# Optimization experiments

Measured on AMD Instinct MI355X. Metric: run time of the kernel, lower is better.

## Reference

```python
import jax, jax.numpy as jnp
import numpy as np

B, S, D = 4, 2048, 512
H, DK = 8, 64
FFN = 2048
LEFT, CHUNK, RIGHT = 512, 128, 128
EPS = 1e-5


def _emformer_mask():
    # True = disallowed. Each query attends to its own chunk, LEFT keys before
    # the chunk start, and RIGHT keys after the chunk end.
    idx = jnp.arange(S)
    cs = (idx // CHUNK) * CHUNK                      # chunk start per query
    j = idx[None, :]
    allowed = (j >= cs[:, None] - LEFT) & (j < cs[:, None] + CHUNK + RIGHT)
    return jnp.broadcast_to(~allowed, (B, 1, S, S))


def _ln(x, g, b):
    m = jnp.mean(x, axis=-1, keepdims=True)
    v = jnp.var(x, axis=-1, keepdims=True)
    return (x - m) * jax.lax.rsqrt(v + EPS) * g + b


def setup_inputs() -> dict:
    key = jax.random.key(0)
    ks = jax.random.split(key, 8)
    w = lambda k, shp: jax.random.normal(k, shp, dtype=jnp.float32) * 0.02
    return {
        "x": jax.random.normal(ks[0], (B, S, D), dtype=jnp.float32),
        "mask": _emformer_mask(),
        "ln_in_g": jnp.ones((D,), jnp.float32), "ln_in_b": jnp.zeros((D,), jnp.float32),
        "wq": w(ks[1], (D, D)), "bq": jnp.zeros((D,), jnp.float32),
        "wk": w(ks[2], (D, D)), "bk": jnp.zeros((D,), jnp.float32),
        "wv": w(ks[3], (D, D)), "bv": jnp.zeros((D,), jnp.float32),
        "ln1_g": jnp.ones((D,), jnp.float32), "ln1_b": jnp.zeros((D,), jnp.float32),
        "w1": w(ks[4], (D, FFN)), "b1": jnp.zeros((FFN,), jnp.float32),
        "w2": w(ks[5], (FFN, D)), "b2": jnp.zeros((D,), jnp.float32),
        "ln2_g": jnp.ones((D,), jnp.float32), "ln2_b": jnp.zeros((D,), jnp.float32),
    }


def reference(x, mask, ln_in_g, ln_in_b, wq, bq, wk, bk, wv, bv,
              ln1_g, ln1_b, w1, b1, w2, b2, ln2_g, ln2_b):
    h = _ln(x, ln_in_g, ln_in_b)                                  # [B,S,D]
    q = (h @ wq + bq).reshape(B, S, H, DK).transpose(0, 2, 1, 3)   # [B,H,S,DK]
    k = (h @ wk + bk).reshape(B, S, H, DK).transpose(0, 2, 1, 3)
    v = (h @ wv + bv).reshape(B, S, H, DK).transpose(0, 2, 1, 3)
    scores = jnp.einsum("bhqd,bhkd->bhqk", q, k) / np.sqrt(DK).astype(np.float32)
    scores = jnp.where(mask, -jnp.inf, scores)
    probs = jax.nn.softmax(scores, axis=-1)
    probs = jnp.where(mask, 0.0, probs)                           # masked_fill after softmax
    out = jnp.einsum("bhqk,bhkd->bhqd", probs, v)
    out = out.transpose(0, 2, 1, 3).reshape(B, S, D)
    attn_out = out + h                                            # residual uses post-LN input
    o = _ln(attn_out, ln1_g, ln1_b)
    o = (o @ w1 + b1) @ w2 + b2 + attn_out                        # NOTE: no activation in source
    return _ln(o, ln2_g, ln2_b)
```

## Files before the change

### kernel.cpp

```cpp
#include <hip/hip_runtime.h>
#include <stdint.h>

#define B_ 4
#define S_ 2048
#define D_ 512
#define H_ 8
#define FFN_ 2048
#define M_ (B_*S_)

typedef unsigned short u16;
typedef __attribute__((ext_vector_type(8))) __bf16 bf16x8;
typedef __attribute__((ext_vector_type(8))) u16 u16x8;
typedef __attribute__((ext_vector_type(4))) u16 u16x4;
typedef __attribute__((ext_vector_type(4))) float f32x4;

__device__ __forceinline__ u16 f2bf(float f) {
  uint32_t u = __builtin_bit_cast(uint32_t, f);
  u += 0x7FFFu + ((u >> 16) & 1u);
  return (u16)(u >> 16);
}
__device__ __forceinline__ bf16x8 ldfrag(const u16* p) {
  return __builtin_bit_cast(bf16x8, *(const u16x8*)p);
}
__device__ __forceinline__ void gld16(const void* g, void* l) {
  __builtin_amdgcn_global_load_lds(
      (const __attribute__((address_space(1))) void*)g,
      (__attribute__((address_space(3))) void*)l, 16, 0, 0);
}
template <int N>
__device__ __forceinline__ void wait_vm_barrier() {
  if constexpr (N == 0)      asm volatile("s_waitcnt vmcnt(0)\n\ts_barrier" ::: "memory");
  else if constexpr (N == 3) asm volatile("s_waitcnt vmcnt(3)\n\ts_barrier" ::: "memory");
  else if constexpr (N == 4) asm volatile("s_waitcnt vmcnt(4)\n\ts_barrier" ::: "memory");
  else if constexpr (N == 6) asm volatile("s_waitcnt vmcnt(6)\n\ts_barrier" ::: "memory");
  else if constexpr (N == 8) asm volatile("s_waitcnt vmcnt(8)\n\ts_barrier" ::: "memory");
}

__global__ __launch_bounds__(256)
void prep(const float* __restrict__ wq, const float* __restrict__ wk,
          const float* __restrict__ wv, const float* __restrict__ w1,
          const float* __restrict__ w2, const float* __restrict__ bq,
          const float* __restrict__ bk, const float* __restrict__ bv,
          u16* __restrict__ wqkvt, u16* __restrict__ w1t,
          u16* __restrict__ w2t, float* __restrict__ bqkv) {
  int id = blockIdx.x, tid = threadIdx.x;
  if (id >= 2816) {
    int i = (id - 2816) * 256 + tid;
    bqkv[i] = i < 512 ? bq[i] : (i < 1024 ? bk[i - 512] : bv[i - 1024]);
    return;
  }
  __shared__ float t[32][33];
  const float* W; u16* dst; int K, N, bx, by;
  if (id < 768) {
    int z = id >> 8, r = id & 255;
    W = z == 0 ? wq : (z == 1 ? wk : wv);
    dst = wqkvt + (size_t)z * 512 * 512; K = 512; N = 512;
    bx = r & 15; by = r >> 4;
  } else if (id < 1792) {
    int r = id - 768; W = w1; dst = w1t; K = 512; N = 2048;
    bx = r & 63; by = r >> 6;
  } else {
    int r = id - 1792; W = w2; dst = w2t; K = 2048; N = 512;
    bx = r & 15; by = r >> 4;
  }
  int n0 = bx * 32, k0 = by * 32, x = tid & 31, y = tid >> 5;
#pragma unroll
  for (int r = 0; r < 4; r++) t[y + 8*r][x] = W[(size_t)(k0 + y + 8*r) * N + n0 + x];
  __syncthreads();
#pragma unroll
  for (int r = 0; r < 4; r++) dst[(size_t)(n0 + y + 8*r) * K + k0 + x] = f2bf(t[x][y + 8*r]);
}

template <bool OUT32, bool OUT16, int NX>
__global__ __launch_bounds__(128)
void ln_k(const float* __restrict__ x, const float* __restrict__ g,
          const float* __restrict__ bta, float* __restrict__ y32,
          u16* __restrict__ y16, const u16* __restrict__ p1,
          const u16* __restrict__ p2, const u16* __restrict__ p3) {
  int row = blockIdx.x;
  int t = threadIdx.x;
  const float* xr = x + (size_t)row * 512;
  f32x4 v = *(const f32x4*)(xr + t * 4);
  if constexpr (NX >= 1) {
    u16x4 a = *(const u16x4*)(p1 + (size_t)row * 512 + t * 4);
#pragma unroll
    for (int j = 0; j < 4; j++) v[j] += __builtin_bit_cast(float, (uint32_t)a[j] << 16);
  }
  if constexpr (NX >= 2) {
    u16x4 a = *(const u16x4*)(p2 + (size_t)row * 512 + t * 4);
#pragma unroll
    for (int j = 0; j < 4; j++) v[j] += __builtin_bit_cast(float, (uint32_t)a[j] << 16);
  }
  if constexpr (NX >= 3) {
    u16x4 a = *(const u16x4*)(p3 + (size_t)row * 512 + t * 4);
#pragma unroll
    for (int j = 0; j < 4; j++) v[j] += __builtin_bit_cast(float, (uint32_t)a[j] << 16);
  }
  float s = v.x + v.y + v.z + v.w;
  float s2 = v.x*v.x + v.y*v.y + v.z*v.z + v.w*v.w;
#pragma unroll
  for (int m = 32; m; m >>= 1) { s += __shfl_xor(s, m); s2 += __shfl_xor(s2, m); }
  __shared__ float p[4];
  int wv = t >> 6;
  if ((t & 63) == 0) { p[wv] = s; p[2 + wv] = s2; }
  __syncthreads();
  s = p[0] + p[1]; s2 = p[2] + p[3];
  float mean = s * (1.f / 512.f);
  float var = s2 * (1.f / 512.f) - mean * mean;
  float rs = rsqrtf(var + 1e-5f);
#pragma unroll
  for (int j = 0; j < 4; j++) {
    float o = (v[j] - mean) * rs * g[t*4 + j] + bta[t*4 + j];
    if constexpr (OUT32) y32[(size_t)row * 512 + t*4 + j] = o;
    if constexpr (OUT16) y16[(size_t)row * 512 + t*4 + j] = f2bf(o);
  }
}

template <int NTW, int NCOL, int KSPLIT, bool RESID, bool OUT32, bool OUT16>
__global__ __launch_bounds__(256)
void gemm_db(const u16* __restrict__ A, const u16* __restrict__ Bt,
             const float* __restrict__ bias, int K, int N,
             const float* resid, float* C32, u16* __restrict__ C16,
             u16* __restrict__ C16b, u16* __restrict__ C16c) {
  __shared__ __align__(16) u16 As[3][128 * 32];
  __shared__ __align__(16) u16 Bs[3][NTW * 1024];
  const int tid = threadIdx.x;
  const int wave = tid >> 6, lane = tid & 63;
  const int l15 = lane & 15, quad = lane >> 4;
  const int wm = wave >> 1, wn = wave & 1;

  int lin = blockIdx.x;
  int kh = 0;
  if constexpr (KSPLIT > 1) {
    const int nblk = (M_ / 128) * NCOL;
    kh = lin / nblk;
    lin -= kh * nblk;
  }
  const int rpx = (M_ / 128) / 8;
  const int xcd = lin & 7, local = lin >> 3;
  const int row0 = (xcd * rpx + local / NCOL) * 128;
  const int col0 = (local % NCOL) * (NTW * 32);
  const int klen = K / KSPLIT;
  const int kstart = kh * klen;

  f32x4 acc[4][NTW];
#pragma unroll
  for (int i = 0; i < 4; i++)
#pragma unroll
    for (int j = 0; j < NTW; j++) acc[i][j] = (f32x4){0.f, 0.f, 0.f, 0.f};

  const int lr = lane >> 2;
  const int lc = ((lane & 3) ^ ((lane >> 3) & 3)) * 8;
  const u16* aG0 = A + (size_t)(row0 + (wave * 2) * 16 + lr) * K + lc;
  const u16* aG1 = A + (size_t)(row0 + (wave * 2 + 1) * 16 + lr) * K + lc;
  const int aO0 = (wave * 2) * 512 + lane * 8;
  const int aO1 = (wave * 2 + 1) * 512 + lane * 8;
  const u16* bG[NTW / 2];
  int bO[NTW / 2];
#pragma unroll
  for (int i = 0; i < NTW / 2; i++) {
    int ch = wave * (NTW / 2) + i;
    bG[i] = Bt + (size_t)(col0 + ch * 16 + lr) * K + lc;
    bO[i] = ch * 512 + lane * 8;
  }
  const int rsw = (l15 >> 1) & 3;
  constexpr int L = 2 + NTW / 2;

  auto issue = [&](int kof, int buf) {
    gld16(aG0 + kof, &As[buf][aO0]);
    gld16(aG1 + kof, &As[buf][aO1]);
#pragma unroll
    for (int i = 0; i < NTW / 2; i++) gld16(bG[i] + kof, &Bs[buf][bO[i]]);
  };

  const int nIter = klen >> 5;
  issue(kstart, 0);
  issue(kstart + 32, 1);

  int cur = 0;
  for (int it = 0; it < nIter; it++) {
    if (it + 1 < nIter) wait_vm_barrier<L>();
    else wait_vm_barrier<0>();
    int pf = cur + 2; if (pf >= 3) pf -= 3;
    if (it + 2 < nIter) issue(kstart + ((it + 2) << 5), pf);
    bf16x8 af[4], bf[NTW];
#pragma unroll
    for (int mt = 0; mt < 4; mt++)
      af[mt] = ldfrag(&As[cur][(wm * 64 + mt * 16 + l15) * 32 + ((quad ^ rsw) * 8)]);
#pragma unroll
    for (int nt = 0; nt < NTW; nt++)
      bf[nt] = ldfrag(&Bs[cur][(wn * (NTW * 16) + nt * 16 + l15) * 32 + ((quad ^ rsw) * 8)]);
#pragma unroll
    for (int mt = 0; mt < 4; mt++)
#pragma unroll
      for (int nt = 0; nt < NTW; nt++)
        acc[mt][nt] = __builtin_amdgcn_mfma_f32_16x16x32_bf16(af[mt], bf[nt], acc[mt][nt], 0, 0, 0);
    cur = cur == 2 ? 0 : cur + 1;
  }
#pragma unroll
  for (int mt = 0; mt < 4; mt++)
#pragma unroll
    for (int nt = 0; nt < NTW; nt++) {
      int n = col0 + wn * (NTW * 16) + nt * 16 + l15;
      float bv = (kh == 0) ? bias[n] : 0.f;
#pragma unroll
      for (int r = 0; r < 4; r++) {
        int m = row0 + wm * 64 + mt * 16 + quad * 4 + r;
        size_t idx = (size_t)m * N + n;
        float val = acc[mt][nt][r] + bv;
        if constexpr (KSPLIT == 4) {
          if (kh == 0)      C32[idx] = val + resid[idx];
          else if (kh == 1) C16[idx] = f2bf(val);
          else if (kh == 2) C16b[idx] = f2bf(val);
          else              C16c[idx] = f2bf(val);
        } else {
          if constexpr (RESID) val += resid[idx];
          if constexpr (OUT32) C32[idx] = val;
          if constexpr (OUT16) C16[idx] = f2bf(val);
        }
      }
    }
}

__global__ __launch_bounds__(256)
void vtrans(const u16* __restrict__ qkv, u16* __restrict__ vt) {
  __shared__ u16 t[64][65];
  int s0 = blockIdx.x * 64, h = blockIdx.y, b = blockIdx.z;
  int x = threadIdx.x, y = threadIdx.y;
  const u16* src = qkv + (size_t)(b * 2048 + s0) * 1536 + 1024 + h * 64;
#pragma unroll
  for (int r = 0; r < 16; r++) { int s = y + 4*r; t[s][x] = src[(size_t)s * 1536 + x]; }
  __syncthreads();
  u16* dst = vt + (size_t)((b * 8 + h) * 64) * 2048 + s0;
#pragma unroll
  for (int r = 0; r < 16; r++) { int d = y + 4*r; dst[(size_t)d * 2048 + x] = t[x][d]; }
}

#define PSTR 136
__global__ __launch_bounds__(256)
void attn_k(const u16* __restrict__ qkv, const u16* __restrict__ vt,
            const float* __restrict__ hres, float* __restrict__ attn) {
  __shared__ __align__(16) u16 smem[8192 + 8192 + 128 * PSTR];
  u16* Ks = smem;
  u16* Vts = smem + 8192;
  u16* Ps = smem + 16384;
  u16* Qs = Ps;

  const int lin = blockIdx.x;
  const int xcd = lin & 7, g = lin >> 3;
  const int c = g & 15;
  const int bh = xcd * 4 + (g >> 4);
  const int hh = bh & 7, b = bh >> 3;
  const int s0 = c * 128;
  const int tid = threadIdx.x, wave = tid >> 6, lane = tid & 63;
  const int l15 = lane & 15, quad = lane >> 4;
  const int t_lo = (c > 4) ? c - 4 : 0;
  const int t_hi = (c + 2 < 16) ? c + 2 : 16;
  const int l7sw = l15 & 7;

  {
    const int cg = ((lane & 7) ^ (lane >> 3)) * 8;
    const int cp = (lane & 7) * 8;
#pragma unroll
    for (int q2 = 0; q2 < 4; q2++) {
      int r = wave * 32 + q2 * 8 + (lane >> 3);
      gld16(qkv + (size_t)(b * 2048 + s0 + r) * 1536 + hh * 64 + cg, Qs + r * 64 + cp);
    }
  }
  __syncthreads();
  bf16x8 qf[2][2];
#pragma unroll
  for (int qg = 0; qg < 2; qg++)
#pragma unroll
    for (int f = 0; f < 2; f++)
      qf[qg][f] = ldfrag(Qs + (qg * 64 + wave * 16 + l15) * 64 + (((f * 4 + quad) ^ l7sw) * 8));

  const u16x8 ones16 = {0x3F80, 0x3F80, 0x3F80, 0x3F80, 0x3F80, 0x3F80, 0x3F80, 0x3F80};
  const bf16x8 onesf = __builtin_bit_cast(bf16x8, ones16);

  f32x4 accO[2][4];
#pragma unroll
  for (int qg = 0; qg < 2; qg++)
#pragma unroll
    for (int i = 0; i < 4; i++) accO[qg][i] = (f32x4){0.f, 0.f, 0.f, 0.f};
  f32x4 accD[2] = {(f32x4){0.f, 0.f, 0.f, 0.f}, (f32x4){0.f, 0.f, 0.f, 0.f}};

  for (int kt = t_lo; kt < t_hi; ++kt) {
    __syncthreads();
    {
      const int cgk = ((lane & 7) ^ (lane >> 3)) * 8;
      const int cpk = (lane & 7) * 8;
#pragma unroll
      for (int q2 = 0; q2 < 4; q2++) {
        int r = wave * 32 + q2 * 8 + (lane >> 3);
        gld16(qkv + (size_t)(b * 2048 + kt * 128 + r) * 1536 + 512 + hh * 64 + cgk,
              Ks + r * 64 + cpk);
      }
      const int cpv = (lane & 15) * 8;
#pragma unroll
      for (int q2 = 0; q2 < 4; q2++) {
        int d = (wave * 4 + q2) * 4 + (lane >> 4);
        int cgv = ((lane & 8) | ((lane & 7) ^ (lane >> 4) ^ ((q2 & 1) << 2))) * 8;
        gld16(vt + (size_t)((b * 8 + hh) * 64 + d) * 2048 + kt * 128 + cgv,
              Vts + d * 128 + cpv);
      }
    }
    __syncthreads();

#pragma unroll
    for (int nt = 0; nt < 8; nt++) {
      bf16x8 kf0 = ldfrag(Ks + (nt * 16 + l15) * 64 + ((quad ^ l7sw) * 8));
      bf16x8 kf1 = ldfrag(Ks + (nt * 16 + l15) * 64 + (((4 + quad) ^ l7sw) * 8));
#pragma unroll
      for (int qg = 0; qg < 2; qg++) {
        f32x4 s4 = (f32x4){0.f, 0.f, 0.f, 0.f};
        s4 = __builtin_amdgcn_mfma_f32_16x16x32_bf16(qf[qg][0], kf0, s4, 0, 0, 0);
        s4 = __builtin_amdgcn_mfma_f32_16x16x32_bf16(qf[qg][1], kf1, s4, 0, 0, 0);
#pragma unroll
        for (int r = 0; r < 4; r++) {
          float pp = exp2f(s4[r] * (1.4426950408889634f * 0.125f));
          Ps[(qg * 64 + wave * 16 + quad * 4 + r) * PSTR + nt * 16 + l15] =
              (u16)(__builtin_bit_cast(uint32_t, pp) >> 16);
        }
      }
    }
#pragma unroll
    for (int ki = 0; ki < 4; ki++) {
      bf16x8 pf[2];
#pragma unroll
      for (int qg = 0; qg < 2; qg++) {
        pf[qg] = ldfrag(Ps + (qg * 64 + wave * 16 + l15) * PSTR + (ki * 4 + quad) * 8);
        accD[qg] = __builtin_amdgcn_mfma_f32_16x16x32_bf16(pf[qg], onesf, accD[qg], 0, 0, 0);
      }
#pragma unroll
      for (int dt = 0; dt < 4; dt++) {
        int gg = ki * 4 + quad;
        bf16x8 vf = ldfrag(Vts + (dt * 16 + l15) * 128 + (((gg & 8) | ((gg & 7) ^ l7sw)) * 8));
#pragma unroll
        for (int qg = 0; qg < 2; qg++)
          accO[qg][dt] = __builtin_amdgcn_mfma_f32_16x16x32_bf16(pf[qg], vf, accO[qg][dt], 0, 0, 0);
      }
    }
  }
#pragma unroll
  for (int qg = 0; qg < 2; qg++)
#pragma unroll
    for (int r = 0; r < 4; r++) {
      float dinv = 1.0f / accD[qg][r];
      int m = s0 + qg * 64 + wave * 16 + quad * 4 + r;
#pragma unroll
      for (int dt = 0; dt < 4; dt++) {
        size_t idx = (size_t)(b * 2048 + m) * 512 + hh * 64 + dt * 16 + l15;
        attn[idx] = accO[qg][dt][r] * dinv + hres[idx];
      }
    }
}

extern "C" void kernel_launch(void* const* d_in, const int* in_sizes, int n_in,
                              void* d_out, int out_size, void* d_ws, size_t ws_size,
                              hipStream_t stream) {
  (void)in_sizes; (void)n_in; (void)out_size; (void)ws_size;
  const float* x       = (const float*)d_in[0];
  const float* ln_in_g = (const float*)d_in[2];
  const float* ln_in_b = (const float*)d_in[3];
  const float* wq = (const float*)d_in[4];
  const float* bq = (const float*)d_in[5];
  const float* wk = (const float*)d_in[6];
  const float* bk = (const float*)d_in[7];
  const float* wv = (const float*)d_in[8];
  const float* bv = (const float*)d_in[9];
  const float* ln1_g = (const float*)d_in[10];
  const float* ln1_b = (const float*)d_in[11];
  const float* w1 = (const float*)d_in[12];
  const float* b1 = (const float*)d_in[13];
  const float* w2 = (const float*)d_in[14];
  const float* b2 = (const float*)d_in[15];
  const float* ln2_g = (const float*)d_in[16];
  const float* ln2_b = (const float*)d_in[17];

  char* ws = (char*)d_ws;
  size_t off = 0;
  auto alloc = [&](size_t bytes) {
    void* p = ws + off;
    off = (off + bytes + 255) & ~(size_t)255;
    return p;
  };
  u16*   wqkvt = (u16*)  alloc((size_t)1536 * 512 * 2);
  float* bqkv  = (float*)alloc(1536 * 4);
  u16*   w1t   = (u16*)  alloc((size_t)2048 * 512 * 2);
  u16*   w2t   = (u16*)  alloc((size_t)512 * 2048 * 2);
  float* h32   = (float*)alloc((size_t)M_ * 512 * 4);
  u16*   h16   = (u16*)  alloc((size_t)M_ * 512 * 2);
  u16*   qkv16 = (u16*)  alloc((size_t)M_ * 1536 * 2);
  u16*   vtb   = (u16*)  alloc((size_t)B_ * H_ * 64 * 2048 * 2);
  float* attn32= (float*)alloc((size_t)M_ * 512 * 4);
  u16*   o16   = h16;
  u16*   f16b  = qkv16;
  u16*   p2b   = (u16*)h32;
  u16*   p3b   = (u16*)h32 + (size_t)M_ * 512;

  prep<<<dim3(2822), 256, 0, stream>>>(wq, wk, wv, w1, w2, bq, bk, bv,
                                       wqkvt, w1t, w2t, bqkv);

  ln_k<true, true, 0><<<M_, 128, 0, stream>>>(x, ln_in_g, ln_in_b, h32, h16,
                                              nullptr, nullptr, nullptr);
  gemm_db<4, 12, 1, false, false, true><<<dim3(12 * 64), 256, 0, stream>>>(
      h16, wqkvt, bqkv, 512, 1536, nullptr, nullptr, qkv16, nullptr, nullptr);
  vtrans<<<dim3(32, 8, 4), dim3(64, 4), 0, stream>>>(qkv16, vtb);
  attn_k<<<dim3(512), 256, 0, stream>>>(qkv16, vtb, h32, attn32);
  ln_k<false, true, 0><<<M_, 128, 0, stream>>>(attn32, ln1_g, ln1_b, nullptr, o16,
                                               nullptr, nullptr, nullptr);
  gemm_db<2, 32, 1, false, false, true><<<dim3(32 * 64), 256, 0, stream>>>(
      o16, w1t, b1, 512, 2048, nullptr, nullptr, f16b, nullptr, nullptr);
  gemm_db<2, 8, 4, false, false, false><<<dim3(4 * 8 * 64), 256, 0, stream>>>(
      f16b, w2t, b2, 2048, 512, attn32, attn32, h16, p2b, p3b);
  ln_k<true, false, 3><<<M_, 128, 0, stream>>>(attn32, ln2_g, ln2_b, (float*)d_out,
                                               nullptr, h16, p2b, p3b);
}
```

Baseline: 290.8 us.

## Replace GEMM kernel with 256x256-tile 8-wave double-buffered MFMA kernel

Swaps the 128-row triple-buffered GEMM for a 256x256 output tile per block using 8 waves and 128KB of dynamic LDS. K steps are 64 wide and double-buffered, and loads for the next stage are interleaved between four quadrant MFMA phases with barriers and s_setprio around the MFMA bursts. The larger tile raises operand reuse and cuts global traffic per flop. The cost is far fewer blocks (192-256, below or near one per CU), which risks poor occupancy and a tail effect, plus a heavy LDS footprint.

```diff
diff --git a/kernel.cpp b/kernel.cpp
--- a/kernel.cpp
+++ b/kernel.cpp
@@ -27,13 +27,25 @@
       (const __attribute__((address_space(1))) void*)g,
       (__attribute__((address_space(3))) void*)l, 16, 0, 0);
 }
+__device__ __forceinline__ void bar() { asm volatile("s_barrier" ::: "memory"); }
 template <int N>
-__device__ __forceinline__ void wait_vm_barrier() {
-  if constexpr (N == 0)      asm volatile("s_waitcnt vmcnt(0)\n\ts_barrier" ::: "memory");
-  else if constexpr (N == 3) asm volatile("s_waitcnt vmcnt(3)\n\ts_barrier" ::: "memory");
-  else if constexpr (N == 4) asm volatile("s_waitcnt vmcnt(4)\n\ts_barrier" ::: "memory");
-  else if constexpr (N == 6) asm volatile("s_waitcnt vmcnt(6)\n\ts_barrier" ::: "memory");
-  else if constexpr (N == 8) asm volatile("s_waitcnt vmcnt(8)\n\ts_barrier" ::: "memory");
+__device__ __forceinline__ void vm_bar() {
+  if constexpr (N == 0) asm volatile("s_waitcnt vmcnt(0)\n\ts_barrier" ::: "memory");
+  else                  asm volatile("s_waitcnt vmcnt(6)\n\ts_barrier" ::: "memory");
+}
+__device__ __forceinline__ void mm16(const bf16x8 (&aF)[4][2],
+                                     const bf16x8 (&bF)[2][2],
+                                     f32x4 (&ac)[4][2]) {
+  __builtin_amdgcn_s_setprio(1);
+#pragma unroll
+  for (int mf = 0; mf < 4; mf++)
+#pragma unroll
+    for (int nf = 0; nf < 2; nf++)
+#pragma unroll
+      for (int ks = 0; ks < 2; ks++)
+        ac[mf][nf] = __builtin_amdgcn_mfma_f32_16x16x32_bf16(
+            aF[mf][ks], bF[nf][ks], ac[mf][nf], 0, 0, 0);
+  __builtin_amdgcn_s_setprio(0);
 }
 
 __global__ __launch_bounds__(256)
@@ -116,110 +128,134 @@
   }
 }
 
-template <int NTW, int NCOL, int KSPLIT, bool RESID, bool OUT32, bool OUT16>
-__global__ __launch_bounds__(256)
-void gemm_db(const u16* __restrict__ A, const u16* __restrict__ Bt,
-             const float* __restrict__ bias, int K, int N,
-             const float* resid, float* C32, u16* __restrict__ C16,
-             u16* __restrict__ C16b, u16* __restrict__ C16c) {
-  __shared__ __align__(16) u16 As[3][128 * 32];
-  __shared__ __align__(16) u16 Bs[3][NTW * 1024];
+template <int KSPLIT, bool RESID, bool OUT32, bool OUT16>
+__global__ __launch_bounds__(512, 2)
+void gemm8(const u16* __restrict__ A, const u16* __restrict__ Bt,
+           const float* __restrict__ bias, int K, int N, int nCol,
+           const float* __restrict__ resid, float* __restrict__ C32,
+           u16* __restrict__ C16, u16* __restrict__ C16b,
+           u16* __restrict__ C16c) {
+  extern __shared__ u16 sm[];
+  u16* Ab = sm;
+  u16* Bb = sm + 32768;
   const int tid = threadIdx.x;
   const int wave = tid >> 6, lane = tid & 63;
-  const int l15 = lane & 15, quad = lane >> 4;
-  const int wm = wave >> 1, wn = wave & 1;
+  const int l15 = lane & 15, quad = lane >> 4, l7 = l15 & 7;
+  const int wm = wave >> 2, wn = wave & 3;
 
   int lin = blockIdx.x;
   int kh = 0;
-  if constexpr (KSPLIT > 1) {
-    const int nblk = (M_ / 128) * NCOL;
-    kh = lin / nblk;
-    lin -= kh * nblk;
-  }
-  const int rpx = (M_ / 128) / 8;
+  const int nblk = 32 * nCol;
+  if constexpr (KSPLIT > 1) { kh = lin / nblk; lin -= kh * nblk; }
   const int xcd = lin & 7, local = lin >> 3;
-  const int row0 = (xcd * rpx + local / NCOL) * 128;
-  const int col0 = (local % NCOL) * (NTW * 32);
-  const int klen = K / KSPLIT;
-  const int kstart = kh * klen;
-
-  f32x4 acc[4][NTW];
-#pragma unroll
-  for (int i = 0; i < 4; i++)
-#pragma unroll
-    for (int j = 0; j < NTW; j++) acc[i][j] = (f32x4){0.f, 0.f, 0.f, 0.f};
-
-  const int lr = lane >> 2;
-  const int lc = ((lane & 3) ^ ((lane >> 3) & 3)) * 8;
-  const u16* aG0 = A + (size_t)(row0 + (wave * 2) * 16 + lr) * K + lc;
-  const u16* aG1 = A + (size_t)(row0 + (wave * 2 + 1) * 16 + lr) * K + lc;
-  const int aO0 = (wave * 2) * 512 + lane * 8;
-  const int aO1 = (wave * 2 + 1) * 512 + lane * 8;
-  const u16* bG[NTW / 2];
-  int bO[NTW / 2];
-#pragma unroll
-  for (int i = 0; i < NTW / 2; i++) {
-    int ch = wave * (NTW / 2) + i;
-    bG[i] = Bt + (size_t)(col0 + ch * 16 + lr) * K + lc;
-    bO[i] = ch * 512 + lane * 8;
-  }
-  const int rsw = (l15 >> 1) & 3;
-  constexpr int L = 2 + NTW / 2;
-
-  auto issue = [&](int kof, int buf) {
-    gld16(aG0 + kof, &As[buf][aO0]);
-    gld16(aG1 + kof, &As[buf][aO1]);
-#pragma unroll
-    for (int i = 0; i < NTW / 2; i++) gld16(bG[i] + kof, &Bs[buf][bO[i]]);
-  };
-
-  const int nIter = klen >> 5;
-  issue(kstart, 0);
-  issue(kstart + 32, 1);
-
-  int cur = 0;
-  for (int it = 0; it < nIter; it++) {
-    if (it + 1 < nIter) wait_vm_barrier<L>();
-    else wait_vm_barrier<0>();
-    int pf = cur + 2; if (pf >= 3) pf -= 3;
-    if (it + 2 < nIter) issue(kstart + ((it + 2) << 5), pf);
-    bf16x8 af[4], bf[NTW];
-#pragma unroll
-    for (int mt = 0; mt < 4; mt++)
-      af[mt] = ldfrag(&As[cur][(wm * 64 + mt * 16 + l15) * 32 + ((quad ^ rsw) * 8)]);
-#pragma unroll
-    for (int nt = 0; nt < NTW; nt++)
-      bf[nt] = ldfrag(&Bs[cur][(wn * (NTW * 16) + nt * 16 + l15) * 32 + ((quad ^ rsw) * 8)]);
-#pragma unroll
-    for (int mt = 0; mt < 4; mt++)
-#pragma unroll
-      for (int nt = 0; nt < NTW; nt++)
-        acc[mt][nt] = __builtin_amdgcn_mfma_f32_16x16x32_bf16(af[mt], bf[nt], acc[mt][nt], 0, 0, 0);
-    cur = cur == 2 ? 0 : cur + 1;
-  }
-#pragma unroll
-  for (int mt = 0; mt < 4; mt++)
-#pragma unroll
-    for (int nt = 0; nt < NTW; nt++) {
-      int n = col0 + wn * (NTW * 16) + nt * 16 + l15;
-      float bv = (kh == 0) ? bias[n] : 0.f;
-#pragma unroll
-      for (int r = 0; r < 4; r++) {
-        int m = row0 + wm * 64 + mt * 16 + quad * 4 + r;
-        size_t idx = (size_t)m * N + n;
-        float val = acc[mt][nt][r] + bv;
-        if constexpr (KSPLIT == 4) {
-          if (kh == 0)      C32[idx] = val + resid[idx];
-          else if (kh == 1) C16[idx] = f2bf(val);
-          else if (kh == 2) C16b[idx] = f2bf(val);
-          else              C16c[idx] = f2bf(val);
-        } else {
-          if constexpr (RESID) val += resid[idx];
-          if constexpr (OUT32) C32[idx] = val;
-          if constexpr (OUT16) C16[idx] = f2bf(val);
+  const int row0 = (xcd * 4 + local / nCol) * 256;
+  const int col0 = (local % nCol) * 256;
+  const int klen = K / KSPLIT, kstart = kh * klen, nT = klen >> 6;
+
+  const int rr = tid >> 3;
+  const int swz = ((tid & 7) ^ (rr & 7)) * 8;
+  const u16* aB = A + (size_t)(row0 + rr) * K + kstart + swz;
+  const u16* bB = Bt + (size_t)(col0 + rr) * K + kstart + swz;
+  const int dOff = tid * 8;
+
+  auto stA = [&](int h, int T, int b) {
+    const u16* s = aB + (size_t)(h * 128) * K + T * 64;
+    u16* d = Ab + b * 16384 + h * 8192 + dOff;
+    gld16(s, d);
+    gld16(s + (size_t)64 * K, d + 4096);
+  };
+  auto stB = [&](int h, int T, int b) {
+    const u16* s = bB + (size_t)(h * 128) * K + T * 64;
+    u16* d = Bb + b * 16384 + h * 8192 + dOff;
+    gld16(s, d);
+    gld16(s + (size_t)64 * K, d + 4096);
+  };
+  auto rdA = [&](int i, int b, bf16x8 (&aF)[4][2]) {
+#pragma unroll
+    for (int mf = 0; mf < 4; mf++)
+#pragma unroll
+      for (int ks = 0; ks < 2; ks++)
+        aF[mf][ks] = ldfrag(Ab + b * 16384 +
+                            (i * 128 + wm * 64 + mf * 16 + l15) * 64 +
+                            (((ks * 4 + quad) ^ l7) * 8));
+  };
+  auto rdB = [&](int j, int b, bf16x8 (&bF)[2][2]) {
+#pragma unroll
+    for (int nf = 0; nf < 2; nf++)
+#pragma unroll
+      for (int ks = 0; ks < 2; ks++)
+        bF[nf][ks] = ldfrag(Bb + b * 16384 +
+                            (j * 128 + wn * 32 + nf * 16 + l15) * 64 +
+                            (((ks * 4 + quad) ^ l7) * 8));
+  };
+
+  f32x4 a00[4][2], a01[4][2], a10[4][2], a11[4][2];
+#pragma unroll
+  for (int mf = 0; mf < 4; mf++)
+#pragma unroll
+    for (int nf = 0; nf < 2; nf++) {
+      a00[mf][nf] = (f32x4){0.f, 0.f, 0.f, 0.f};
+      a01[mf][nf] = (f32x4){0.f, 0.f, 0.f, 0.f};
+      a10[mf][nf] = (f32x4){0.f, 0.f, 0.f, 0.f};
+      a11[mf][nf] = (f32x4){0.f, 0.f, 0.f, 0.f};
+    }
+
+  stA(0, 0, 0); stB(0, 0, 0); stB(1, 0, 0); stA(1, 0, 0);
+  stA(0, 1, 1); stB(0, 1, 1); stB(1, 1, 1);
+  vm_bar<6>();
+
+  bf16x8 aF[4][2], bF0[2][2], bF1[2][2];
+  for (int t = 0; t < nT; ++t) {
+    const int b = t & 1;
+    rdA(0, b, aF); rdB(0, b, bF0);
+    if (t + 1 < nT) stA(1, t + 1, b ^ 1);
+    bar();
+    mm16(aF, bF0, a00);
+    bar();
+    rdB(1, b, bF1);
+    if (t + 2 < nT) stA(0, t + 2, b);
+    bar();
+    mm16(aF, bF1, a01);
+    bar();
+    rdA(1, b, aF);
+    if (t + 2 < nT) stB(0, t + 2, b);
+    bar();
+    mm16(aF, bF0, a10);
+    bar();
+    if (t + 2 < nT) stB(1, t + 2, b);
+    bar();
+    mm16(aF, bF1, a11);
+    if (t + 2 < nT) vm_bar<6>();
+    else if (t + 1 < nT) vm_bar<0>();
+    else bar();
+  }
+
+  auto wrQ = [&](int i, int j, f32x4 (&ac)[4][2]) {
+#pragma unroll
+    for (int mf = 0; mf < 4; mf++)
+#pragma unroll
+      for (int nf = 0; nf < 2; nf++) {
+        const int n = col0 + j * 128 + wn * 32 + nf * 16 + l15;
+        const float bv = (kh == 0) ? bias[n] : 0.f;
+#pragma unroll
+        for (int r = 0; r < 4; r++) {
+          const int m = row0 + i * 128 + wm * 64 + mf * 16 + quad * 4 + r;
+          const size_t idx = (size_t)m * N + n;
+          float val = ac[mf][nf][r] + bv;
+          if constexpr (KSPLIT == 4) {
+            if (kh == 0)      C32[idx] = val + resid[idx];
+            else if (kh == 1) C16[idx] = f2bf(val);
+            else if (kh == 2) C16b[idx] = f2bf(val);
+            else              C16c[idx] = f2bf(val);
+          } else {
+            if constexpr (RESID) val += resid[idx];
+            if constexpr (OUT32) C32[idx] = val;
+            if constexpr (OUT16) C16[idx] = f2bf(val);
+          }
         }
       }
-    }
+  };
+  wrQ(0, 0, a00); wrQ(0, 1, a01); wrQ(1, 0, a10); wrQ(1, 1, a11);
 }
 
 __global__ __launch_bounds__(256)
@@ -398,22 +434,32 @@
   u16*   f16b  = qkv16;
   u16*   p2b   = (u16*)h32;
   u16*   p3b   = (u16*)h32 + (size_t)M_ * 512;
+  (void)vtb;
+
+  static bool attrSet = false;
+  if (!attrSet) {
+    hipFuncSetAttribute(reinterpret_cast<const void*>(&gemm8<1, false, false, true>),
+                        hipFuncAttributeMaxDynamicSharedMemorySize, 131072);
+    hipFuncSetAttribute(reinterpret_cast<const void*>(&gemm8<4, false, false, false>),
+                        hipFuncAttributeMaxDynamicSharedMemorySize, 131072);
+    attrSet = true;
+  }
 
   prep<<<dim3(2822), 256, 0, stream>>>(wq, wk, wv, w1, w2, bq, bk, bv,
                                        wqkvt, w1t, w2t, bqkv);
 
   ln_k<true, true, 0><<<M_, 128, 0, stream>>>(x, ln_in_g, ln_in_b, h32, h16,
                                               nullptr, nullptr, nullptr);
-  gemm_db<4, 12, 1, false, false, true><<<dim3(12 * 64), 256, 0, stream>>>(
-      h16, wqkvt, bqkv, 512, 1536, nullptr, nullptr, qkv16, nullptr, nullptr);
+  gemm8<1, false, false, true><<<dim3(192), 512, 131072, stream>>>(
+      h16, wqkvt, bqkv, 512, 1536, 6, nullptr, nullptr, qkv16, nullptr, nullptr);
   vtrans<<<dim3(32, 8, 4), dim3(64, 4), 0, stream>>>(qkv16, vtb);
   attn_k<<<dim3(512), 256, 0, stream>>>(qkv16, vtb, h32, attn32);
   ln_k<false, true, 0><<<M_, 128, 0, stream>>>(attn32, ln1_g, ln1_b, nullptr, o16,
                                                nullptr, nullptr, nullptr);
-  gemm_db<2, 32, 1, false, false, true><<<dim3(32 * 64), 256, 0, stream>>>(
-      o16, w1t, b1, 512, 2048, nullptr, nullptr, f16b, nullptr, nullptr);
-  gemm_db<2, 8, 4, false, false, false><<<dim3(4 * 8 * 64), 256, 0, stream>>>(
-      f16b, w2t, b2, 2048, 512, attn32, attn32, h16, p2b, p3b);
+  gemm8<1, false, false, true><<<dim3(256), 512, 131072, stream>>>(
+      o16, w1t, b1, 512, 2048, 8, nullptr, nullptr, f16b, nullptr, nullptr);
+  gemm8<4, false, false, false><<<dim3(256), 512, 131072, stream>>>(
+      f16b, w2t, b2, 2048, 512, 2, attn32, attn32, h16, p2b, p3b);
   ln_k<true, false, 3><<<M_, 128, 0, stream>>>(attn32, ln2_g, ln2_b, (float*)d_out,
                                                nullptr, h16, p2b, p3b);
 }
```

New measurement: 307.1 us. 5.6% more time.

## Switch GEMM to double-buffered LDS pipeline and retune tile widths and occupancy

Applied to the files above, without the earlier changes.

Replaces the three-stage global-to-LDS prefetch ring, which used explicit vmcnt waits, with a two-buffer scheme synchronized by __syncthreads each k-step. LDS use drops and a minimum-waves launch bound is added to raise occupancy. Tile widths per GEMM are swapped: QKV uses narrower N tiles with more blocks, FFN GEMMs use wider tiles with fewer blocks. The shallower pipeline may expose more load latency per iteration.

```diff
diff --git a/kernel.cpp b/kernel.cpp
--- a/kernel.cpp
+++ b/kernel.cpp
@@ -26,14 +26,6 @@
   __builtin_amdgcn_global_load_lds(
       (const __attribute__((address_space(1))) void*)g,
       (__attribute__((address_space(3))) void*)l, 16, 0, 0);
-}
-template <int N>
-__device__ __forceinline__ void wait_vm_barrier() {
-  if constexpr (N == 0)      asm volatile("s_waitcnt vmcnt(0)\n\ts_barrier" ::: "memory");
-  else if constexpr (N == 3) asm volatile("s_waitcnt vmcnt(3)\n\ts_barrier" ::: "memory");
-  else if constexpr (N == 4) asm volatile("s_waitcnt vmcnt(4)\n\ts_barrier" ::: "memory");
-  else if constexpr (N == 6) asm volatile("s_waitcnt vmcnt(6)\n\ts_barrier" ::: "memory");
-  else if constexpr (N == 8) asm volatile("s_waitcnt vmcnt(8)\n\ts_barrier" ::: "memory");
 }
 
 __global__ __launch_bounds__(256)
@@ -116,14 +108,14 @@
   }
 }
 
-template <int NTW, int NCOL, int KSPLIT, bool RESID, bool OUT32, bool OUT16>
-__global__ __launch_bounds__(256)
+template <int NTW, int NCOL, int KSPLIT, bool RESID, bool OUT32, bool OUT16, int MINW>
+__global__ __launch_bounds__(256, MINW)
 void gemm_db(const u16* __restrict__ A, const u16* __restrict__ Bt,
              const float* __restrict__ bias, int K, int N,
              const float* resid, float* C32, u16* __restrict__ C16,
              u16* __restrict__ C16b, u16* __restrict__ C16c) {
-  __shared__ __align__(16) u16 As[3][128 * 32];
-  __shared__ __align__(16) u16 Bs[3][NTW * 1024];
+  __shared__ __align__(16) u16 As[2][128 * 32];
+  __shared__ __align__(16) u16 Bs[2][NTW * 1024];
   const int tid = threadIdx.x;
   const int wave = tid >> 6, lane = tid & 63;
   const int l15 = lane & 15, quad = lane >> 4;
@@ -164,7 +156,6 @@
     bO[i] = ch * 512 + lane * 8;
   }
   const int rsw = (l15 >> 1) & 3;
-  constexpr int L = 2 + NTW / 2;
 
   auto issue = [&](int kof, int buf) {
     gld16(aG0 + kof, &As[buf][aO0]);
@@ -175,14 +166,11 @@
 
   const int nIter = klen >> 5;
   issue(kstart, 0);
-  issue(kstart + 32, 1);
-
-  int cur = 0;
+  __syncthreads();
+
   for (int it = 0; it < nIter; it++) {
-    if (it + 1 < nIter) wait_vm_barrier<L>();
-    else wait_vm_barrier<0>();
-    int pf = cur + 2; if (pf >= 3) pf -= 3;
-    if (it + 2 < nIter) issue(kstart + ((it + 2) << 5), pf);
+    const int cur = it & 1;
+    if (it + 1 < nIter) issue(kstart + ((it + 1) << 5), cur ^ 1);
     bf16x8 af[4], bf[NTW];
 #pragma unroll
     for (int mt = 0; mt < 4; mt++)
@@ -195,7 +183,7 @@
 #pragma unroll
       for (int nt = 0; nt < NTW; nt++)
         acc[mt][nt] = __builtin_amdgcn_mfma_f32_16x16x32_bf16(af[mt], bf[nt], acc[mt][nt], 0, 0, 0);
-    cur = cur == 2 ? 0 : cur + 1;
+    __syncthreads();
   }
 #pragma unroll
   for (int mt = 0; mt < 4; mt++)
@@ -404,15 +392,15 @@
 
   ln_k<true, true, 0><<<M_, 128, 0, stream>>>(x, ln_in_g, ln_in_b, h32, h16,
                                               nullptr, nullptr, nullptr);
-  gemm_db<4, 12, 1, false, false, true><<<dim3(12 * 64), 256, 0, stream>>>(
+  gemm_db<2, 24, 1, false, false, true, 6><<<dim3(24 * 64), 256, 0, stream>>>(
       h16, wqkvt, bqkv, 512, 1536, nullptr, nullptr, qkv16, nullptr, nullptr);
   vtrans<<<dim3(32, 8, 4), dim3(64, 4), 0, stream>>>(qkv16, vtb);
   attn_k<<<dim3(512), 256, 0, stream>>>(qkv16, vtb, h32, attn32);
   ln_k<false, true, 0><<<M_, 128, 0, stream>>>(attn32, ln1_g, ln1_b, nullptr, o16,
                                                nullptr, nullptr, nullptr);
-  gemm_db<2, 32, 1, false, false, true><<<dim3(32 * 64), 256, 0, stream>>>(
+  gemm_db<4, 16, 1, false, false, true, 5><<<dim3(16 * 64), 256, 0, stream>>>(
       o16, w1t, b1, 512, 2048, nullptr, nullptr, f16b, nullptr, nullptr);
-  gemm_db<2, 8, 4, false, false, false><<<dim3(4 * 8 * 64), 256, 0, stream>>>(
+  gemm_db<4, 4, 4, false, false, false, 5><<<dim3(4 * 4 * 64), 256, 0, stream>>>(
       f16b, w2t, b2, 2048, 512, attn32, attn32, h16, p2b, p3b);
   ln_k<true, false, 3><<<M_, 128, 0, stream>>>(attn32, ln2_g, ln2_b, (float*)d_out,
                                                nullptr, h16, p2b, p3b);
```

After: 295.4 us. About the same (+1.6%).
